# Performance work log

Hardware: AMD Instinct MI355X
Metric: run time of the kernel (lower is better)

## Reference

```python
import jax, jax.numpy as jnp
import numpy as np

EPS = 1e-12  # matches torch F.normalize eps


def setup_inputs() -> dict:
    key = jax.random.key(0)
    k1, k2 = jax.random.split(key)
    N, D, K = 262144, 128, 512
    embeddings = jax.random.normal(k1, (N, D), dtype=jnp.float32)
    init_centroids = jax.random.normal(k2, (K, D), dtype=jnp.float32)
    return {"embeddings": embeddings, "init_centroids": init_centroids, "num_iters": 5}


def _kmeans_iter(centroids, embeddings, K):
    # [N, K] similarity, hard assignment by argmax (k-means E-step with dot-product metric)
    dots = jnp.matmul(embeddings, centroids.T)
    assign = jnp.argmax(dots, axis=1)  # [N] int32
    # M-step: per-cluster sum + counts (replaces CPU dict-of-lists + python loop)
    emb_sums = jax.ops.segment_sum(embeddings, assign, num_segments=K)  # [K, D]
    counts = jax.ops.segment_sum(jnp.ones(embeddings.shape[0], dtype=embeddings.dtype),
                                 assign, num_segments=K)  # [K]
    # only update clusters with members (mask = counts > 0), keep old centroid otherwise
    new_c = jnp.where(counts[:, None] > 0,
                      emb_sums / jnp.maximum(counts, 1.0)[:, None],
                      centroids)
    # F.normalize(dim=1, p=2) applied to ALL centroids
    norm = jnp.maximum(jnp.linalg.norm(new_c, axis=1, keepdims=True), EPS)
    return new_c / norm, assign


def reference(embeddings, init_centroids, num_iters):
    K = init_centroids.shape[0]
    centroids = init_centroids
    assign = jnp.zeros(embeddings.shape[0], dtype=jnp.int32)
    for _ in range(num_iters):  # small static iteration count (k-means iters)
        centroids, assign = _kmeans_iter(centroids, embeddings, K)
    return assign, centroids
```

## Files before the change

### kernel.cpp

```cpp
#include <hip/hip_runtime.h>

#define NN 262144
#define DD 128
#define KK 512
#define NITER 5

#define SKH 136

#define SE 132
#define SC 260
#define SS 129

#define DELTA 2e-3f

#define WS_A16_BYTES   (NN * 2)
#define WS_SUMS_OFF    (WS_A16_BYTES)
#define WS_CNTS_OFF    (WS_SUMS_OFF + 2048 * DD * 4)
#define WS_NEEDED      (WS_CNTS_OFF + 2048 * 4)
#define WS_CH_OFF      (WS_SUMS_OFF + NN)
#define WS_CL_OFF      (WS_CH_OFF + KK * DD * 2)
#define WS_EAB3_OFF    (WS_NEEDED)
#define WS_EAB3_BYTES  (NN * DD * 4)
#define WS_NEEDED2     (WS_EAB3_OFF + WS_EAB3_BYTES)

using s8     = __attribute__((ext_vector_type(8))) short;
using f32x4  = __attribute__((ext_vector_type(4))) float;
using f32x16 = __attribute__((ext_vector_type(16))) float;

__device__ __forceinline__ unsigned f2bf(float x) {
    unsigned u = __float_as_uint(x);
    return (u + 0x7fffu + ((u >> 16) & 1u)) >> 16;
}

__device__ __forceinline__ void split4(float4 v, uint2& h, uint2& s) {
    unsigned hx = f2bf(v.x), hy = f2bf(v.y), hz = f2bf(v.z), hw = f2bf(v.w);
    float rx = v.x - __uint_as_float(hx << 16);
    float ry = v.y - __uint_as_float(hy << 16);
    float rz = v.z - __uint_as_float(hz << 16);
    float rw = v.w - __uint_as_float(hw << 16);
    unsigned lx = f2bf(rx), ly = f2bf(ry), lz = f2bf(rz), lw = f2bf(rw);
    h.x = hx | (hy << 16); h.y = hz | (hw << 16);
    s.x = lx | (ly << 16); s.y = lz | (lw << 16);
}

__global__ __launch_bounds__(256) void presplit_e3_kernel(
    const float* __restrict__ E, unsigned short* __restrict__ EAB)
{
    const int u   = blockIdx.x * 4 + (threadIdx.x >> 6);
    const int l   = threadIdx.x & 63;
    const int g32 = u >> 3, ks = u & 7;
    const int row = g32 * 32 + (l & 31);
    const int k0  = ks * 16 + (l >> 5) * 8;
    float4 v0 = *(const float4*)&E[(size_t)row * DD + k0];
    float4 v1 = *(const float4*)&E[(size_t)row * DD + k0 + 4];
    uint2 h0, s0, h1, s1;
    split4(v0, h0, s0); split4(v1, h1, s1);
    size_t base = (size_t)u * 2048 + l * 16;
    *(uint2*)((char*)EAB + base)        = h0;
    *(uint2*)((char*)EAB + base + 8)    = h1;
    *(uint2*)((char*)EAB + base + 1024) = s0;
    *(uint2*)((char*)EAB + base + 1032) = s1;
}

__global__ __launch_bounds__(256) void split_c3_kernel(
    const float* __restrict__ C, unsigned short* __restrict__ CH,
    unsigned short* __restrict__ CL)
{
    int idx = blockIdx.x * 256 + threadIdx.x;
    int col = idx >> 5;
    int k4  = (idx & 31) << 2;
    float4 v = *(const float4*)&C[(size_t)col * DD + k4];
    uint2 h, s;
    split4(v, h, s);
    int unit = (col >> 5) * 8 + (k4 >> 4);
    int lane = (col & 31) + ((k4 >> 3) & 1) * 32;
    int off  = unit * 512 + lane * 8 + (k4 & 7);
    *(uint2*)&CH[off] = h;
    *(uint2*)&CL[off] = s;
}

__global__ __launch_bounds__(256, 2) void assign5_kernel(
    const unsigned short* __restrict__ EAB,
    const unsigned short* __restrict__ CH, const unsigned short* __restrict__ CL,
    int* __restrict__ assignv, unsigned short* __restrict__ assign16,
    unsigned char* __restrict__ flags)
{
    __shared__ char bld[2][32768];

    const int tid = threadIdx.x;
    const int l   = tid & 63;
    const int wid = tid >> 6;
    const int j   = l & 31;
    const int h   = l >> 5;
    const int r0  = blockIdx.x * 128;
    const int g32 = blockIdx.x * 4 + wid;

    const char* Abase = (const char*)EAB + (size_t)g32 * 16384 + l * 16;
    s8 Ah[8], Al[8];
#pragma unroll
    for (int ks = 0; ks < 8; ++ks) {
        Ah[ks] = *(const s8*)(Abase + ks * 2048);
        Al[ks] = *(const s8*)(Abase + ks * 2048 + 1024);
    }

    float bv[16], sv[16];
    int   bk[16];
#pragma unroll
    for (int i = 0; i < 16; ++i) { bv[i] = -3.4e38f; sv[i] = -3.4e38f; bk[i] = 0; }

    {
        uint4 rH[4], rL[4];
#pragma unroll
        for (int p = 0; p < 4; ++p) {
            rH[p] = *(const uint4*)((const char*)CH + (p * 256 + tid) * 16);
            rL[p] = *(const uint4*)((const char*)CL + (p * 256 + tid) * 16);
        }
#pragma unroll
        for (int p = 0; p < 4; ++p) {
            *(uint4*)(bld[0] + (p * 256 + tid) * 16)         = rH[p];
            *(uint4*)(bld[0] + 16384 + (p * 256 + tid) * 16) = rL[p];
        }
    }
    __syncthreads();

#pragma unroll
    for (int hc = 0; hc < 8; ++hc) {
        const int cur = hc & 1, nxt = cur ^ 1;

        uint4 rH[4], rL[4];
        if (hc < 7) {
            const char* srcH = (const char*)CH + (hc + 1) * 16384;
            const char* srcL = (const char*)CL + (hc + 1) * 16384;
#pragma unroll
            for (int p = 0; p < 4; ++p) {
                rH[p] = *(const uint4*)(srcH + (p * 256 + tid) * 16);
                rL[p] = *(const uint4*)(srcL + (p * 256 + tid) * 16);
            }
        }

        f32x16 acc[2];
#pragma unroll
        for (int cfi = 0; cfi < 2; ++cfi)
#pragma unroll
            for (int r = 0; r < 16; ++r) acc[cfi][r] = 0.f;

#pragma unroll
        for (int ks = 0; ks < 8; ++ks) {
#pragma unroll
            for (int cfi = 0; cfi < 2; ++cfi) {
                const int uu = cfi * 8 + ks;
                s8 bh = *(const s8*)(bld[cur] + uu * 1024 + l * 16);
                s8 bl = *(const s8*)(bld[cur] + 16384 + uu * 1024 + l * 16);
                acc[cfi] = __builtin_amdgcn_mfma_f32_32x32x16_bf16(
                    Ah[ks], bh, acc[cfi], 0, 0, 0);
                acc[cfi] = __builtin_amdgcn_mfma_f32_32x32x16_bf16(
                    Ah[ks], bl, acc[cfi], 0, 0, 0);
                acc[cfi] = __builtin_amdgcn_mfma_f32_32x32x16_bf16(
                    Al[ks], bh, acc[cfi], 0, 0, 0);
            }
        }

#pragma unroll
        for (int cfi = 0; cfi < 2; ++cfi) {
            const int kg = hc * 64 + cfi * 32 + j;
#pragma unroll
            for (int r = 0; r < 16; ++r) {
                float v = acc[cfi][r];
                if (v > bv[r]) { sv[r] = bv[r]; bv[r] = v; bk[r] = kg; }
                else           { sv[r] = fmaxf(sv[r], v); }
            }
        }

        if (hc < 7) {
#pragma unroll
            for (int p = 0; p < 4; ++p) {
                *(uint4*)(bld[nxt] + (p * 256 + tid) * 16)         = rH[p];
                *(uint4*)(bld[nxt] + 16384 + (p * 256 + tid) * 16) = rL[p];
            }
            __syncthreads();
        }
    }

#pragma unroll
    for (int r = 0; r < 16; ++r) {
        float v1 = bv[r], v2 = sv[r]; int k1 = bk[r];
#pragma unroll
        for (int m = 1; m <= 16; m <<= 1) {
            float ov = __shfl_xor(v1, m, 64);
            float os = __shfl_xor(v2, m, 64);
            int   ok = __shfl_xor(k1, m, 64);
            if (ov > v1) { v2 = fmaxf(v1, os); v1 = ov; k1 = ok; }
            else         { v2 = fmaxf(v2, ov); }
        }
        bv[r] = v1; sv[r] = v2; bk[r] = k1;
    }

#pragma unroll
    for (int r = 0; r < 16; ++r) {
        if (j == r) {
            int rowg = r0 + wid * 32 + (r & 3) + 8 * (r >> 2) + 4 * h;
            assignv[rowg]  = bk[r];
            assign16[rowg] = (unsigned short)bk[r];
            flags[rowg]    = (bv[r] - sv[r] < DELTA) ? 1 : 0;
        }
    }
}

__global__ __launch_bounds__(512) void update_partial3_kernel(
    const float* __restrict__ E, const unsigned short* __restrict__ assign16,
    float* __restrict__ ws_sums, int* __restrict__ ws_cnts)
{
    const int b   = blockIdx.x;
    const int k   = b >> 2;
    const int qtr = b & 3;

    __shared__ float acc[8][DD];
    __shared__ int   cnts[8];

    const int tid  = threadIdx.x;
    const int w    = tid >> 6;
    const int lane = tid & 63;

    float a0 = 0.f, a1 = 0.f;
    int cnt = 0;
    const int wbase = qtr * (NN / 4) + w * (NN / 32);

    for (int it = 0; it < (NN / 32) / 512; ++it) {
        const int off = wbase + it * 512;
        uint4 p = *(const uint4*)&assign16[off + lane * 8];
        unsigned v[4] = {p.x, p.y, p.z, p.w};
#pragma unroll
        for (int h = 0; h < 4; ++h) {
            int lo = (int)(v[h] & 0xffffu);
            int hi = (int)(v[h] >> 16);
            unsigned long long mlo = __ballot(lo == k);
            unsigned long long mhi = __ballot(hi == k);
            cnt += (int)__popcll(mlo) + (int)__popcll(mhi);
            while (mlo) {
                int b2 = __ffsll((long long)mlo) - 1; mlo &= mlo - 1;
                int row = off + b2 * 8 + h * 2;
                float2 e = *(const float2*)&E[(size_t)row * DD + lane * 2];
                a0 += e.x; a1 += e.y;
            }
            while (mhi) {
                int b2 = __ffsll((long long)mhi) - 1; mhi &= mhi - 1;
                int row = off + b2 * 8 + h * 2 + 1;
                float2 e = *(const float2*)&E[(size_t)row * DD + lane * 2];
                a0 += e.x; a1 += e.y;
            }
        }
    }
    acc[w][lane * 2]     = a0;
    acc[w][lane * 2 + 1] = a1;
    if (lane == 0) cnts[w] = cnt;
    __syncthreads();
    if (tid < DD) {
        float s = acc[0][tid] + acc[1][tid] + acc[2][tid] + acc[3][tid]
                + acc[4][tid] + acc[5][tid] + acc[6][tid] + acc[7][tid];
        ws_sums[(size_t)b * DD + tid] = s;
    }
    if (tid == 0)
        ws_cnts[b] = cnts[0] + cnts[1] + cnts[2] + cnts[3]
                   + cnts[4] + cnts[5] + cnts[6] + cnts[7];
}

__global__ __launch_bounds__(256) void split_c_kernel(
    const float* __restrict__ C, unsigned short* __restrict__ CH,
    unsigned short* __restrict__ CL)
{
    int idx = blockIdx.x * 256 + threadIdx.x;
    int col = idx >> 5;
    int k4  = (idx & 31) << 2;
    float4 v = *(const float4*)&C[(size_t)col * DD + k4];
    uint2 h, s;
    split4(v, h, s);
    int group = (col >> 4) * 4 + (k4 >> 5);
    int inner = ((k4 >> 3) & 3) * 16 + (col & 15);
    int off   = group * 512 + inner * 8 + (k4 & 7);
    *(uint2*)&CH[off] = h;
    *(uint2*)&CL[off] = s;
}

__global__ __launch_bounds__(256, 2) void assign_kernel(
    const float* __restrict__ E,
    const unsigned short* __restrict__ CH, const unsigned short* __restrict__ CL,
    int* __restrict__ assignv, unsigned short* __restrict__ assign16,
    unsigned char* __restrict__ flags)
{
    __shared__ unsigned short lds[2 * 128 * SKH];
    unsigned short* EH = lds;
    unsigned short* EL = lds + 128 * SKH;

    const int tid = threadIdx.x;
    const int l   = tid & 63;
    const int wid = tid >> 6;
    const int wr  = wid >> 1;
    const int wc  = wid & 1;
    const int c   = l & 15;
    const int g   = l >> 4;
    const int r0  = blockIdx.x * 128;

#pragma unroll
    for (int it = 0; it < 16; ++it) {
        int idx = it * 256 + tid;
        int row = idx >> 5;
        int k4  = (idx & 31) << 2;
        float4 v = *(const float4*)&E[(size_t)(r0 + row) * DD + k4];
        uint2 h, s;
        split4(v, h, s);
        *(uint2*)&EH[row * SKH + k4] = h;
        *(uint2*)&EL[row * SKH + k4] = s;
    }
    __syncthreads();

    float bv[16], sv[16];
    int   bk[16];
#pragma unroll
    for (int i = 0; i < 16; ++i) { bv[i] = -3.4e38f; sv[i] = -3.4e38f; bk[i] = 0; }

    const int aoff0 = (wr * 64 + c) * SKH + g * 8;
    const int bbase = wc * 16 * 512 + l * 8;

    s8 bh[2][4], bl[2][4];
#pragma unroll
    for (int cf = 0; cf < 4; ++cf) {
        int off = bbase + (cf * 4) * 512;
        bh[0][cf] = *(const s8*)&CH[off];
        bl[0][cf] = *(const s8*)&CL[off];
    }

    f32x4 acc[4][4];

#pragma unroll
    for (int t = 0; t < 16; ++t) {
        const int cc  = t >> 2, kc = t & 3;
        const int cur = t & 1,  nxt = cur ^ 1;

        if (kc == 0) {
#pragma unroll
            for (int rf = 0; rf < 4; ++rf)
#pragma unroll
                for (int cf = 0; cf < 4; ++cf)
                    acc[rf][cf] = (f32x4){0.f, 0.f, 0.f, 0.f};
        }

        if (t < 15) {
            const int t1 = t + 1, cc1 = t1 >> 2, kc1 = t1 & 3;
#pragma unroll
            for (int cf = 0; cf < 4; ++cf) {
                int off = bbase + (cc1 * 32 + cf * 4 + kc1) * 512;
                bh[nxt][cf] = *(const s8*)&CH[off];
                bl[nxt][cf] = *(const s8*)&CL[off];
            }
        }

        s8 ah[4], al[4];
#pragma unroll
        for (int rf = 0; rf < 4; ++rf) {
            int off = aoff0 + rf * 16 * SKH + kc * 32;
            ah[rf] = *(const s8*)&EH[off];
            al[rf] = *(const s8*)&EL[off];
        }

#pragma unroll
        for (int rf = 0; rf < 4; ++rf)
#pragma unroll
            for (int cf = 0; cf < 4; ++cf) {
                acc[rf][cf] = __builtin_amdgcn_mfma_f32_16x16x32_bf16(
                    ah[rf], bh[cur][cf], acc[rf][cf], 0, 0, 0);
                acc[rf][cf] = __builtin_amdgcn_mfma_f32_16x16x32_bf16(
                    ah[rf], bl[cur][cf], acc[rf][cf], 0, 0, 0);
                acc[rf][cf] = __builtin_amdgcn_mfma_f32_16x16x32_bf16(
                    al[rf], bh[cur][cf], acc[rf][cf], 0, 0, 0);
            }

        if (kc == 3) {
            const int kbase = cc * 128 + wc * 64 + c;
#pragma unroll
            for (int rf = 0; rf < 4; ++rf)
#pragma unroll
                for (int i = 0; i < 4; ++i) {
                    const int sidx = rf * 4 + i;
#pragma unroll
                    for (int cf = 0; cf < 4; ++cf) {
                        float v = acc[rf][cf][i];
                        int  kg = kbase + cf * 16;
                        if (v > bv[sidx]) { sv[sidx] = bv[sidx]; bv[sidx] = v; bk[sidx] = kg; }
                        else              { sv[sidx] = fmaxf(sv[sidx], v); }
                    }
                }
        }
    }

#pragma unroll
    for (int s = 0; s < 16; ++s) {
        float v1 = bv[s], v2 = sv[s]; int k1 = bk[s];
#pragma unroll
        for (int m = 1; m <= 8; m <<= 1) {
            float ov = __shfl_xor(v1, m, 64);
            float os = __shfl_xor(v2, m, 64);
            int   ok = __shfl_xor(k1, m, 64);
            if (ov > v1) { v2 = fmaxf(v1, os); v1 = ov; k1 = ok; }
            else         { v2 = fmaxf(v2, ov); }
        }
        bv[s] = v1; sv[s] = v2; bk[s] = k1;
    }

    __syncthreads();
    float* mv = (float*)lds;
    int*   mk = (int*)lds + 256;
    float* ms = (float*)lds + 512;
    if (c == 0) {
#pragma unroll
        for (int rf = 0; rf < 4; ++rf)
#pragma unroll
            for (int i = 0; i < 4; ++i) {
                int row = wr * 64 + rf * 16 + g * 4 + i;
                mv[wc * 128 + row] = bv[rf * 4 + i];
                mk[wc * 128 + row] = bk[rf * 4 + i];
                ms[wc * 128 + row] = sv[rf * 4 + i];
            }
    }
    __syncthreads();
    if (tid < 128) {
        float v1 = mv[tid], v2 = ms[tid]; int k1 = mk[tid];
        float ov = mv[128 + tid], os = ms[128 + tid]; int ok = mk[128 + tid];
        if (ov > v1) { v2 = fmaxf(v1, os); v1 = ov; k1 = ok; }
        else         { v2 = fmaxf(v2, ov); }
        assignv[r0 + tid] = k1;
        assign16[r0 + tid] = (unsigned short)k1;
        flags[r0 + tid] = (v1 - v2 < DELTA) ? 1 : 0;
    }
}

__global__ __launch_bounds__(256) void rescue_kernel(
    const float* __restrict__ E, const float* __restrict__ C,
    const unsigned char* __restrict__ flags,
    int* __restrict__ assignv, unsigned short* __restrict__ assign16)
{
    __shared__ int   rows[128];
    __shared__ int   nf;
    __shared__ float ev[DD];
    __shared__ float rv[4];
    __shared__ int   rk[4];

    const int tid  = threadIdx.x;
    const int base = blockIdx.x * 128;

    if (tid == 0) nf = 0;
    __syncthreads();
    if (tid < 128 && flags[base + tid]) {
        int p = atomicAdd(&nf, 1);
        rows[p] = base + tid;
    }
    __syncthreads();
    const int n = nf;
    if (n == 0) return;

    for (int i = 0; i < n; ++i) {
        const int row = rows[i];
        if (tid < 32)
            *(float4*)&ev[tid * 4] = *(const float4*)&E[(size_t)row * DD + tid * 4];
        __syncthreads();

        float d0 = 0.f, d1 = 0.f;
        for (int q = 0; q < 32; ++q) {
            float4 e4 = *(const float4*)&ev[q * 4];
            float4 c0 = *(const float4*)&C[(size_t)tid * DD + q * 4];
            float4 c1 = *(const float4*)&C[(size_t)(tid + 256) * DD + q * 4];
            d0 = fmaf(e4.x, c0.x, d0); d0 = fmaf(e4.y, c0.y, d0);
            d0 = fmaf(e4.z, c0.z, d0); d0 = fmaf(e4.w, c0.w, d0);
            d1 = fmaf(e4.x, c1.x, d1); d1 = fmaf(e4.y, c1.y, d1);
            d1 = fmaf(e4.z, c1.z, d1); d1 = fmaf(e4.w, c1.w, d1);
        }
        float v = (d0 >= d1) ? d0 : d1;
        int   k = (d0 >= d1) ? tid : tid + 256;
#pragma unroll
        for (int m = 1; m <= 32; m <<= 1) {
            float ov = __shfl_xor(v, m, 64);
            int   ok = __shfl_xor(k, m, 64);
            if (ov > v || (ov == v && ok < k)) { v = ov; k = ok; }
        }
        if ((tid & 63) == 0) { rv[tid >> 6] = v; rk[tid >> 6] = k; }
        __syncthreads();
        if (tid == 0) {
            float bv2 = rv[0]; int bk2 = rk[0];
#pragma unroll
            for (int w = 1; w < 4; ++w)
                if (rv[w] > bv2 || (rv[w] == bv2 && rk[w] < bk2)) { bv2 = rv[w]; bk2 = rk[w]; }
            assignv[row] = bk2;
            assign16[row] = (unsigned short)bk2;
        }
        __syncthreads();
    }
}

__global__ __launch_bounds__(256, 2) void assign_valu_kernel(
    const float* __restrict__ E, const float* __restrict__ C,
    int* __restrict__ assignv, unsigned short* __restrict__ assign16)
{
    __shared__ float smem[32 * SE + 32 * SC];
    float* ET = smem;
    float* CT = smem + 32 * SE;
    float* sval = smem;
    int*   sidx = ((int*)smem) + 32 * SS;

    const int tid = threadIdx.x;
    const int tx  = tid & 31;
    const int ty  = tid >> 5;
    const int r0  = blockIdx.x * 128;

    float bbv = 0.f;
    int   bbk = 0;

    for (int chunk = 0; chunk < 2; ++chunk) {
        const int k0 = chunk * 256;
        float acc[16][8];
#pragma unroll
        for (int i = 0; i < 16; ++i)
#pragma unroll
            for (int j = 0; j < 8; ++j) acc[i][j] = 0.f;

        for (int sub = 0; sub < 4; ++sub) {
            const int d0 = sub * 32;
            __syncthreads();
#pragma unroll
            for (int it = 0; it < 4; ++it) {
                int idx = tid + it * 256;
                int r = idx >> 3, q = idx & 7;
                float4 v = *(const float4*)&E[(r0 + r) * DD + d0 + q * 4];
                ET[(q * 4 + 0) * SE + r] = v.x;
                ET[(q * 4 + 1) * SE + r] = v.y;
                ET[(q * 4 + 2) * SE + r] = v.z;
                ET[(q * 4 + 3) * SE + r] = v.w;
            }
#pragma unroll
            for (int it = 0; it < 8; ++it) {
                int idx = tid + it * 256;
                int k = idx >> 3, q = idx & 7;
                float4 v = *(const float4*)&C[(k0 + k) * DD + d0 + q * 4];
                CT[(q * 4 + 0) * SC + k] = v.x;
                CT[(q * 4 + 1) * SC + k] = v.y;
                CT[(q * 4 + 2) * SC + k] = v.z;
                CT[(q * 4 + 3) * SC + k] = v.w;
            }
            __syncthreads();
#pragma unroll 4
            for (int d = 0; d < 32; ++d) {
                float4 a0 = *(const float4*)&ET[d * SE + ty * 16];
                float4 a1 = *(const float4*)&ET[d * SE + ty * 16 + 4];
                float4 a2 = *(const float4*)&ET[d * SE + ty * 16 + 8];
                float4 a3 = *(const float4*)&ET[d * SE + ty * 16 + 12];
                float4 b0 = *(const float4*)&CT[d * SC + tx * 4];
                float4 b1 = *(const float4*)&CT[d * SC + 128 + tx * 4];
                float ra[16] = {a0.x, a0.y, a0.z, a0.w, a1.x, a1.y, a1.z, a1.w,
                                a2.x, a2.y, a2.z, a2.w, a3.x, a3.y, a3.z, a3.w};
                float rb[8]  = {b0.x, b0.y, b0.z, b0.w, b1.x, b1.y, b1.z, b1.w};
#pragma unroll
                for (int i = 0; i < 16; ++i)
#pragma unroll
                    for (int j = 0; j < 8; ++j)
                        acc[i][j] = fmaf(ra[i], rb[j], acc[i][j]);
            }
        }
        __syncthreads();

#pragma unroll
        for (int i = 0; i < 16; ++i) {
            float bv = acc[i][0]; int bj = 0;
#pragma unroll
            for (int j = 1; j < 8; ++j)
                if (acc[i][j] > bv) { bv = acc[i][j]; bj = j; }
            int row = ty * 16 + i;
            int gk = k0 + ((bj < 4) ? (tx * 4 + bj) : (128 + tx * 4 + (bj - 4)));
            sval[tx * SS + row] = bv;
            sidx[tx * SS + row] = gk;
        }
        __syncthreads();
        if (tid < 128) {
            float bv = sval[tid]; int bi = sidx[tid];
            for (int t = 1; t < 32; ++t) {
                float v = sval[t * SS + tid];
                int   x = sidx[t * SS + tid];
                if (v > bv || (v == bv && x < bi)) { bv = v; bi = x; }
            }
            if (chunk == 0 || bv > bbv || (bv == bbv && bi < bbk)) {
                bbv = bv; bbk = bi;
            }
        }
    }
    if (tid < 128) {
        assignv[r0 + tid] = bbk;
        if (assign16) assign16[r0 + tid] = (unsigned short)bbk;
    }
}

__global__ __launch_bounds__(256) void update_partial_kernel(
    const float* __restrict__ E, const unsigned short* __restrict__ assign16,
    float* __restrict__ ws_sums, int* __restrict__ ws_cnts)
{
    const int b   = blockIdx.x;
    const int k   = b >> 2;
    const int qtr = b & 3;

    __shared__ float acc[4][DD];
    __shared__ int   cnts[4];

    const int tid  = threadIdx.x;
    const int w    = tid >> 6;
    const int lane = tid & 63;

    float a0 = 0.f, a1 = 0.f;
    int cnt = 0;
    const int wbase = qtr * (NN / 4) + w * (NN / 16);

    for (int it = 0; it < (NN / 16) / 512; ++it) {
        const int off = wbase + it * 512;
        uint4 p = *(const uint4*)&assign16[off + lane * 8];
        unsigned v[4] = {p.x, p.y, p.z, p.w};
#pragma unroll
        for (int h = 0; h < 4; ++h) {
            int lo = (int)(v[h] & 0xffffu);
            int hi = (int)(v[h] >> 16);
            unsigned long long mlo = __ballot(lo == k);
            unsigned long long mhi = __ballot(hi == k);
            cnt += (int)__popcll(mlo) + (int)__popcll(mhi);
            while (mlo) {
                int b2 = __ffsll((long long)mlo) - 1; mlo &= mlo - 1;
                int row = off + b2 * 8 + h * 2;
                float2 e = *(const float2*)&E[(size_t)row * DD + lane * 2];
                a0 += e.x; a1 += e.y;
            }
            while (mhi) {
                int b2 = __ffsll((long long)mhi) - 1; mhi &= mhi - 1;
                int row = off + b2 * 8 + h * 2 + 1;
                float2 e = *(const float2*)&E[(size_t)row * DD + lane * 2];
                a0 += e.x; a1 += e.y;
            }
        }
    }
    acc[w][lane * 2]     = a0;
    acc[w][lane * 2 + 1] = a1;
    if (lane == 0) cnts[w] = cnt;
    __syncthreads();
    if (tid < DD)
        ws_sums[(size_t)b * DD + tid] = acc[0][tid] + acc[1][tid] + acc[2][tid] + acc[3][tid];
    if (tid == 0)
        ws_cnts[b] = cnts[0] + cnts[1] + cnts[2] + cnts[3];
}

__global__ __launch_bounds__(128) void update_combine_kernel(
    const float* __restrict__ ws_sums, const int* __restrict__ ws_cnts,
    float* __restrict__ C)
{
    const int k = blockIdx.x, t = threadIdx.x;
    __shared__ float red[2];
    const int w = t >> 6, lane = t & 63;

    float s = ws_sums[(size_t)(4 * k + 0) * DD + t]
            + ws_sums[(size_t)(4 * k + 1) * DD + t]
            + ws_sums[(size_t)(4 * k + 2) * DD + t]
            + ws_sums[(size_t)(4 * k + 3) * DD + t];
    int cnt = ws_cnts[4 * k] + ws_cnts[4 * k + 1] + ws_cnts[4 * k + 2] + ws_cnts[4 * k + 3];
    float m = (cnt > 0) ? s / (float)cnt : C[k * DD + t];

    float sq = m * m;
#pragma unroll
    for (int o = 32; o > 0; o >>= 1) sq += __shfl_down(sq, o, 64);
    if (lane == 0) red[w] = sq;
    __syncthreads();
    float nrm = fmaxf(sqrtf(red[0] + red[1]), 1e-12f);
    C[k * DD + t] = m / nrm;
}

__global__ __launch_bounds__(256) void update_kernel(
    const float* __restrict__ E, const int* __restrict__ assignv,
    float* __restrict__ C)
{
    const int k = blockIdx.x;
    __shared__ float acc[4][DD];
    __shared__ int   cnts[4];
    __shared__ float red[4];

    const int tid  = threadIdx.x;
    const int w    = tid >> 6;
    const int lane = tid & 63;

    float a0 = 0.f, a1 = 0.f;
    int cnt = 0;
    const int per_wave = NN / 4;
    const int base = w * per_wave;

    for (int it = 0; it < per_wave / 256; ++it) {
        const int off = base + it * 256;
        int4 as = *(const int4*)&assignv[off + lane * 4];
        int av[4] = {as.x, as.y, as.z, as.w};
#pragma unroll
        for (int ci = 0; ci < 4; ++ci) {
            unsigned long long m = __ballot(av[ci] == k);
            cnt += (int)__popcll(m);
            while (m) {
                int b = __ffsll((long long)m) - 1;
                m &= m - 1;
                int r = off + b * 4 + ci;
                float2 v = *(const float2*)&E[r * DD + lane * 2];
                a0 += v.x; a1 += v.y;
            }
        }
    }
    acc[w][lane * 2]     = a0;
    acc[w][lane * 2 + 1] = a1;
    if (lane == 0) cnts[w] = cnt;
    __syncthreads();

    float m = 0.f;
    const int ctot = cnts[0] + cnts[1] + cnts[2] + cnts[3];
    if (tid < DD) {
        float s = acc[0][tid] + acc[1][tid] + acc[2][tid] + acc[3][tid];
        m = (ctot > 0) ? s / (float)ctot : C[k * DD + tid];
    }
    float sq = m * m;
#pragma unroll
    for (int o = 32; o > 0; o >>= 1) sq += __shfl_down(sq, o, 64);
    if (lane == 0) red[w] = sq;
    __syncthreads();
    if (tid < DD) {
        float nrm = fmaxf(sqrtf(red[0] + red[1]), 1e-12f);
        C[k * DD + tid] = m / nrm;
    }
}

__global__ void finalize_kernel(float* __restrict__ out)
{
    int i = blockIdx.x * 256 + threadIdx.x;
    if (i < NN) {
        int a = ((const int*)out)[i];
        out[i] = (float)a;
    }
}

extern "C" void kernel_launch(void* const* d_in, const int* in_sizes, int n_in,
                              void* d_out, int out_size, void* d_ws, size_t ws_size,
                              hipStream_t stream)
{
    (void)in_sizes; (void)n_in; (void)out_size;

    const float* E  = (const float*)d_in[0];
    const float* C0 = (const float*)d_in[1];

    float* out     = (float*)d_out;
    float* C       = out + NN;
    int*   assignv = (int*)out;

    const bool fast  = (ws_size >= (size_t)WS_NEEDED);
    const bool fast2 = (ws_size >= (size_t)WS_NEEDED2);
    unsigned short* assign16 = fast ? (unsigned short*)d_ws : nullptr;
    float* ws_sums = fast ? (float*)((char*)d_ws + WS_SUMS_OFF) : nullptr;
    int*   ws_cnts = fast ? (int*)((char*)d_ws + WS_CNTS_OFF) : nullptr;
    unsigned char* flags = fast ? (unsigned char*)d_ws + WS_SUMS_OFF : nullptr;
    unsigned short* CH = fast ? (unsigned short*)((char*)d_ws + WS_CH_OFF) : nullptr;
    unsigned short* CL = fast ? (unsigned short*)((char*)d_ws + WS_CL_OFF) : nullptr;
    unsigned short* EAB = fast2 ? (unsigned short*)((char*)d_ws + WS_EAB3_OFF) : nullptr;

    hipMemcpyAsync(C, C0, (size_t)KK * DD * sizeof(float),
                   hipMemcpyDeviceToDevice, stream);

    if (fast2)
        presplit_e3_kernel<<<16384, 256, 0, stream>>>(E, EAB);

    for (int it = 0; it < NITER; ++it) {
        if (fast2) {
            split_c3_kernel<<<KK * DD / 4 / 256, 256, 0, stream>>>(C, CH, CL);
            assign5_kernel<<<NN / 128, 256, 0, stream>>>(EAB, CH, CL,
                                                         assignv, assign16, flags);
            rescue_kernel<<<NN / 128, 256, 0, stream>>>(E, C, flags, assignv, assign16);
            update_partial3_kernel<<<2048, 512, 0, stream>>>(E, assign16, ws_sums, ws_cnts);
            update_combine_kernel<<<KK, 128, 0, stream>>>(ws_sums, ws_cnts, C);
        } else if (fast) {
            split_c_kernel<<<KK * DD / 4 / 256, 256, 0, stream>>>(C, CH, CL);
            assign_kernel<<<NN / 128, 256, 0, stream>>>(E, CH, CL, assignv, assign16, flags);
            rescue_kernel<<<NN / 128, 256, 0, stream>>>(E, C, flags, assignv, assign16);
            update_partial_kernel<<<2048, 256, 0, stream>>>(E, assign16, ws_sums, ws_cnts);
            update_combine_kernel<<<KK, 128, 0, stream>>>(ws_sums, ws_cnts, C);
        } else {
            assign_valu_kernel<<<NN / 128, 256, 0, stream>>>(E, C, assignv, nullptr);
            update_kernel<<<KK, 256, 0, stream>>>(E, assignv, C);
        }
    }
    finalize_kernel<<<(NN + 255) / 256, 256, 0, stream>>>(out);
}
```

Before: 1.263 ms.

## Replace scan-based cluster update with histogram, scan, scatter and list-driven sums

```diff
diff --git a/kernel.cpp b/kernel.cpp
--- a/kernel.cpp
+++ b/kernel.cpp
@@ -12,6 +12,9 @@
 #define SS 129
 
 #define DELTA 2e-3f
+
+#define FXS 16777216.0f
+#define FXI (1.0 / 16777216.0)
 
 #define WS_A16_BYTES   (NN * 2)
 #define WS_SUMS_OFF    (WS_A16_BYTES)
@@ -22,6 +25,11 @@
 #define WS_EAB3_OFF    (WS_NEEDED)
 #define WS_EAB3_BYTES  (NN * DD * 4)
 #define WS_NEEDED2     (WS_EAB3_OFF + WS_EAB3_BYTES)
+#define WS_LIST_OFF    (WS_NEEDED2)
+#define WS_CNT_OFF     (WS_LIST_OFF + NN * 4)
+#define WS_CURS_OFF    (WS_CNT_OFF + 2048)
+#define WS_OFF_OFF     (WS_CURS_OFF + 2048)
+#define WS_NEEDED3     (WS_OFF_OFF + 2048)
 
 using s8     = __attribute__((ext_vector_type(8))) short;
 using f32x4  = __attribute__((ext_vector_type(4))) float;
@@ -206,6 +214,94 @@
     }
 }
 
+__global__ __launch_bounds__(256) void hist_kernel(
+    const unsigned short* __restrict__ assign16, int* __restrict__ cnt)
+{
+    __shared__ int h[KK];
+    const int tid = threadIdx.x;
+    for (int i = tid; i < KK; i += 256) h[i] = 0;
+    __syncthreads();
+    uint2 p = *(const uint2*)&assign16[blockIdx.x * 1024 + tid * 4];
+    atomicAdd(&h[p.x & 0xffffu], 1);
+    atomicAdd(&h[p.x >> 16], 1);
+    atomicAdd(&h[p.y & 0xffffu], 1);
+    atomicAdd(&h[p.y >> 16], 1);
+    __syncthreads();
+    for (int i = tid; i < KK; i += 256)
+        if (h[i]) atomicAdd(&cnt[i], h[i]);
+}
+
+__global__ __launch_bounds__(512) void scan_kernel(
+    const int* __restrict__ cnt, int* __restrict__ offv)
+{
+    __shared__ int sh[KK];
+    const int t = threadIdx.x;
+    const int v = cnt[t];
+    sh[t] = v;
+    __syncthreads();
+    for (int d = 1; d < KK; d <<= 1) {
+        int x = (t >= d) ? sh[t - d] : 0;
+        __syncthreads();
+        sh[t] += x;
+        __syncthreads();
+    }
+    offv[t] = sh[t] - v;
+}
+
+__global__ __launch_bounds__(512) void scatter_kernel(
+    const unsigned short* __restrict__ assign16, const int* __restrict__ offv,
+    int* __restrict__ cursor, int* __restrict__ list)
+{
+    const int r = blockIdx.x * 512 + threadIdx.x;
+    const int k = assign16[r];
+    const int pos = atomicAdd(&cursor[k], 1);
+    list[offv[k] + pos] = r;
+}
+
+__global__ __launch_bounds__(256) void psum_kernel(
+    const float* __restrict__ E, const int* __restrict__ list,
+    const int* __restrict__ cnt, const int* __restrict__ offv,
+    float* __restrict__ ws_sums, int* __restrict__ ws_cnts)
+{
+    __shared__ long long red[16][DD];
+
+    const int b   = blockIdx.x;
+    const int k   = b >> 2;
+    const int qtr = b & 3;
+    const int tid = threadIdx.x;
+    const int s   = tid >> 4;
+    const int d0  = (tid & 15) * 8;
+
+    const int ck = cnt[k], ob = offv[k];
+    const int qs = ob + ((ck * qtr) >> 2);
+    const int qe = ob + ((ck * (qtr + 1)) >> 2);
+
+    long long a[8] = {0, 0, 0, 0, 0, 0, 0, 0};
+    for (int i = qs + s; i < qe; i += 16) {
+        const int r = list[i];
+        float4 v0 = *(const float4*)&E[(size_t)r * DD + d0];
+        float4 v1 = *(const float4*)&E[(size_t)r * DD + d0 + 4];
+        a[0] += (long long)llrintf(v0.x * FXS);
+        a[1] += (long long)llrintf(v0.y * FXS);
+        a[2] += (long long)llrintf(v0.z * FXS);
+        a[3] += (long long)llrintf(v0.w * FXS);
+        a[4] += (long long)llrintf(v1.x * FXS);
+        a[5] += (long long)llrintf(v1.y * FXS);
+        a[6] += (long long)llrintf(v1.z * FXS);
+        a[7] += (long long)llrintf(v1.w * FXS);
+    }
+#pragma unroll
+    for (int j = 0; j < 8; ++j) red[s][d0 + j] = a[j];
+    __syncthreads();
+    if (tid < DD) {
+        long long x = 0;
+#pragma unroll
+        for (int s2 = 0; s2 < 16; ++s2) x += red[s2][tid];
+        ws_sums[(size_t)b * DD + tid] = (float)((double)x * FXI);
+    }
+    if (tid == 0) ws_cnts[b] = qe - qs;
+}
+
 __global__ __launch_bounds__(512) void update_partial3_kernel(
     const float* __restrict__ E, const unsigned short* __restrict__ assign16,
     float* __restrict__ ws_sums, int* __restrict__ ws_cnts)
@@ -754,6 +850,7 @@
 
     const bool fast  = (ws_size >= (size_t)WS_NEEDED);
     const bool fast2 = (ws_size >= (size_t)WS_NEEDED2);
+    const bool fast3 = (ws_size >= (size_t)WS_NEEDED3);
     unsigned short* assign16 = fast ? (unsigned short*)d_ws : nullptr;
     float* ws_sums = fast ? (float*)((char*)d_ws + WS_SUMS_OFF) : nullptr;
     int*   ws_cnts = fast ? (int*)((char*)d_ws + WS_CNTS_OFF) : nullptr;
@@ -761,6 +858,10 @@
     unsigned short* CH = fast ? (unsigned short*)((char*)d_ws + WS_CH_OFF) : nullptr;
     unsigned short* CL = fast ? (unsigned short*)((char*)d_ws + WS_CL_OFF) : nullptr;
     unsigned short* EAB = fast2 ? (unsigned short*)((char*)d_ws + WS_EAB3_OFF) : nullptr;
+    int* list   = fast3 ? (int*)((char*)d_ws + WS_LIST_OFF) : nullptr;
+    int* cnt    = fast3 ? (int*)((char*)d_ws + WS_CNT_OFF) : nullptr;
+    int* cursor = fast3 ? (int*)((char*)d_ws + WS_CURS_OFF) : nullptr;
+    int* offv   = fast3 ? (int*)((char*)d_ws + WS_OFF_OFF) : nullptr;
 
     hipMemcpyAsync(C, C0, (size_t)KK * DD * sizeof(float),
                    hipMemcpyDeviceToDevice, stream);
@@ -774,7 +875,15 @@
             assign5_kernel<<<NN / 128, 256, 0, stream>>>(EAB, CH, CL,
                                                          assignv, assign16, flags);
             rescue_kernel<<<NN / 128, 256, 0, stream>>>(E, C, flags, assignv, assign16);
-            update_partial3_kernel<<<2048, 512, 0, stream>>>(E, assign16, ws_sums, ws_cnts);
+            if (fast3) {
+                hipMemsetAsync(cnt, 0, 4096, stream);
+                hist_kernel<<<NN / 1024, 256, 0, stream>>>(assign16, cnt);
+                scan_kernel<<<1, 512, 0, stream>>>(cnt, offv);
+                scatter_kernel<<<NN / 512, 512, 0, stream>>>(assign16, offv, cursor, list);
+                psum_kernel<<<2048, 256, 0, stream>>>(E, list, cnt, offv, ws_sums, ws_cnts);
+            } else {
+                update_partial3_kernel<<<2048, 512, 0, stream>>>(E, assign16, ws_sums, ws_cnts);
+            }
             update_combine_kernel<<<KK, 128, 0, stream>>>(ws_sums, ws_cnts, C);
         } else if (fast) {
             split_c_kernel<<<KK * DD / 4 / 256, 256, 0, stream>>>(C, CH, CL);
```

After: 1.646 ms. 30.3% more time.

## Halve centroid LDS chunk to raise occupancy in assign kernel

Applied to the files above, without the earlier changes.

```diff
diff --git a/kernel.cpp b/kernel.cpp
--- a/kernel.cpp
+++ b/kernel.cpp
@@ -79,13 +79,13 @@
     *(uint2*)&CL[off] = s;
 }
 
-__global__ __launch_bounds__(256, 2) void assign5_kernel(
+__global__ __launch_bounds__(256, 4) void assign5_kernel(
     const unsigned short* __restrict__ EAB,
     const unsigned short* __restrict__ CH, const unsigned short* __restrict__ CL,
     int* __restrict__ assignv, unsigned short* __restrict__ assign16,
     unsigned char* __restrict__ flags)
 {
-    __shared__ char bld[2][32768];
+    __shared__ char bld[2][16384];
 
     const int tid = threadIdx.x;
     const int l   = tid & 63;
@@ -109,73 +109,63 @@
     for (int i = 0; i < 16; ++i) { bv[i] = -3.4e38f; sv[i] = -3.4e38f; bk[i] = 0; }
 
     {
-        uint4 rH[4], rL[4];
-#pragma unroll
-        for (int p = 0; p < 4; ++p) {
+        uint4 rH[2], rL[2];
+#pragma unroll
+        for (int p = 0; p < 2; ++p) {
             rH[p] = *(const uint4*)((const char*)CH + (p * 256 + tid) * 16);
             rL[p] = *(const uint4*)((const char*)CL + (p * 256 + tid) * 16);
         }
 #pragma unroll
-        for (int p = 0; p < 4; ++p) {
-            *(uint4*)(bld[0] + (p * 256 + tid) * 16)         = rH[p];
-            *(uint4*)(bld[0] + 16384 + (p * 256 + tid) * 16) = rL[p];
-        }
-    }
-    __syncthreads();
-
-#pragma unroll
-    for (int hc = 0; hc < 8; ++hc) {
-        const int cur = hc & 1, nxt = cur ^ 1;
-
-        uint4 rH[4], rL[4];
-        if (hc < 7) {
-            const char* srcH = (const char*)CH + (hc + 1) * 16384;
-            const char* srcL = (const char*)CL + (hc + 1) * 16384;
-#pragma unroll
-            for (int p = 0; p < 4; ++p) {
+        for (int p = 0; p < 2; ++p) {
+            *(uint4*)(bld[0] + (p * 256 + tid) * 16)        = rH[p];
+            *(uint4*)(bld[0] + 8192 + (p * 256 + tid) * 16) = rL[p];
+        }
+    }
+    __syncthreads();
+
+#pragma unroll
+    for (int qc = 0; qc < 16; ++qc) {
+        const int cur = qc & 1, nxt = cur ^ 1;
+
+        uint4 rH[2], rL[2];
+        if (qc < 15) {
+            const char* srcH = (const char*)CH + (qc + 1) * 8192;
+            const char* srcL = (const char*)CL + (qc + 1) * 8192;
+#pragma unroll
+            for (int p = 0; p < 2; ++p) {
                 rH[p] = *(const uint4*)(srcH + (p * 256 + tid) * 16);
                 rL[p] = *(const uint4*)(srcL + (p * 256 + tid) * 16);
             }
         }
 
-        f32x16 acc[2];
-#pragma unroll
-        for (int cfi = 0; cfi < 2; ++cfi)
-#pragma unroll
-            for (int r = 0; r < 16; ++r) acc[cfi][r] = 0.f;
+        f32x16 acc;
+#pragma unroll
+        for (int r = 0; r < 16; ++r) acc[r] = 0.f;
 
 #pragma unroll
         for (int ks = 0; ks < 8; ++ks) {
-#pragma unroll
-            for (int cfi = 0; cfi < 2; ++cfi) {
-                const int uu = cfi * 8 + ks;
-                s8 bh = *(const s8*)(bld[cur] + uu * 1024 + l * 16);
-                s8 bl = *(const s8*)(bld[cur] + 16384 + uu * 1024 + l * 16);
-                acc[cfi] = __builtin_amdgcn_mfma_f32_32x32x16_bf16(
-                    Ah[ks], bh, acc[cfi], 0, 0, 0);
-                acc[cfi] = __builtin_amdgcn_mfma_f32_32x32x16_bf16(
-                    Ah[ks], bl, acc[cfi], 0, 0, 0);
-                acc[cfi] = __builtin_amdgcn_mfma_f32_32x32x16_bf16(
-                    Al[ks], bh, acc[cfi], 0, 0, 0);
-            }
-        }
-
-#pragma unroll
-        for (int cfi = 0; cfi < 2; ++cfi) {
-            const int kg = hc * 64 + cfi * 32 + j;
+            s8 bh = *(const s8*)(bld[cur] + ks * 1024 + l * 16);
+            s8 bl = *(const s8*)(bld[cur] + 8192 + ks * 1024 + l * 16);
+            acc = __builtin_amdgcn_mfma_f32_32x32x16_bf16(Ah[ks], bh, acc, 0, 0, 0);
+            acc = __builtin_amdgcn_mfma_f32_32x32x16_bf16(Ah[ks], bl, acc, 0, 0, 0);
+            acc = __builtin_amdgcn_mfma_f32_32x32x16_bf16(Al[ks], bh, acc, 0, 0, 0);
+        }
+
+        {
+            const int kg = qc * 32 + j;
 #pragma unroll
             for (int r = 0; r < 16; ++r) {
-                float v = acc[cfi][r];
+                float v = acc[r];
                 if (v > bv[r]) { sv[r] = bv[r]; bv[r] = v; bk[r] = kg; }
                 else           { sv[r] = fmaxf(sv[r], v); }
             }
         }
 
-        if (hc < 7) {
-#pragma unroll
-            for (int p = 0; p < 4; ++p) {
-                *(uint4*)(bld[nxt] + (p * 256 + tid) * 16)         = rH[p];
-                *(uint4*)(bld[nxt] + 16384 + (p * 256 + tid) * 16) = rL[p];
+        if (qc < 15) {
+#pragma unroll
+            for (int p = 0; p < 2; ++p) {
+                *(uint4*)(bld[nxt] + (p * 256 + tid) * 16)        = rH[p];
+                *(uint4*)(bld[nxt] + 8192 + (p * 256 + tid) * 16) = rL[p];
             }
             __syncthreads();
         }
```

Measured after the change: 2.359 ms. +86.7%, slower.
